# Kernel tuning notes

Hardware: AMD Instinct MI355X
Metric: run time of the kernel (lower is better)

## Reference

```python
import jax, jax.numpy as jnp
import numpy as np

EPS = 1e-5

def _conv(x, w, pad):
    # NCHW / OIHW 2-D convolution, stride 1
    return jax.lax.conv_general_dilated(
        x, w, window_strides=(1, 1), padding=[(pad, pad), (pad, pad)],
        dimension_numbers=('NCHW', 'OIHW', 'NCHW'))

def _bn2d(x, g, b, m, v):
    inv = g * jax.lax.rsqrt(v + EPS)
    return x * inv[None, :, None, None] + (b - m * inv)[None, :, None, None]

def _bn1d(x, g, b, m, v):
    inv = g * jax.lax.rsqrt(v + EPS)
    return x * inv[None, :] + (b - m * inv)[None, :]

def _avgpool2(x):
    B, C, H, W = x.shape
    return x.reshape(B, C, H // 2, 2, W // 2, 2).mean(axis=(3, 5))

def _hardtanh01(x):
    return jnp.clip(x, 0.0, 1.0)

def setup_inputs() -> dict:
    key = jax.random.key(0)
    ks = jax.random.split(key, 24)
    B = 1024
    d = {}
    d['x_in'] = jax.random.normal(ks[0], (B, 3, 32, 32), dtype=jnp.float32)
    d['w1'] = jax.random.normal(ks[1], (32, 3, 5, 5), dtype=jnp.float32) * 0.1
    d['w2'] = jax.random.normal(ks[2], (32, 32, 5, 5), dtype=jnp.float32) * 0.05
    d['w3'] = jax.random.normal(ks[3], (64, 32, 5, 5), dtype=jnp.float32) * 0.05
    d['w4'] = jax.random.normal(ks[4], (10, 64, 4, 4), dtype=jnp.float32) * 0.05
    for i, (c, k0) in enumerate([(32, 5), (32, 9), (64, 13), (10, 17)], start=1):
        d[f'g{i}'] = jax.random.uniform(ks[k0], (c,), minval=0.5, maxval=1.5, dtype=jnp.float32)
        d[f'b{i}'] = jax.random.normal(ks[k0 + 1], (c,), dtype=jnp.float32) * 0.1
        d[f'm{i}'] = jax.random.normal(ks[k0 + 2], (c,), dtype=jnp.float32) * 0.1
        d[f'v{i}'] = jax.random.uniform(ks[k0 + 3], (c,), minval=0.5, maxval=1.5, dtype=jnp.float32)
    return d

def reference(x_in, w1, w2, w3, w4,
              g1, b1, m1, v1, g2, b2, m2, v2,
              g3, b3, m3, v3, g4, b4, m4, v4):
    # conv1 -> bn1 -> pool -> hardtanh(0,1)
    x = _hardtanh01(_avgpool2(_bn2d(_conv(x_in, w1, 2), g1, b1, m1, v1)))
    # conv2 -> bn2 -> pool -> hardtanh(0,1)
    x = _hardtanh01(_avgpool2(_bn2d(_conv(x, w2, 2), g2, b2, m2, v2)))
    # conv3 -> bn3 -> pool -> hardtanh(0,1)
    x = _hardtanh01(_avgpool2(_bn2d(_conv(x, w3, 2), g3, b3, m3, v3)))
    # fc1 as 4x4 conv, valid padding -> (B, num_classes, 1, 1)
    x = _conv(x, w4, 0).reshape(x.shape[0], -1)
    return _bn1d(x, g4, b4, m4, v4)
```

## Files before the change

kernel.cpp:

```cpp
#include <hip/hip_runtime.h>

#define EPSF 1e-5f

typedef _Float16 half8 __attribute__((ext_vector_type(8)));
typedef _Float16 half4v __attribute__((ext_vector_type(4)));
typedef float f32x4 __attribute__((ext_vector_type(4)));

__device__ __forceinline__ float clamp01(float x){ return fminf(fmaxf(x, 0.f), 1.f); }

__global__ __launch_bounds__(256) void k_prep(
    const float* __restrict__ w1, const float* __restrict__ w2,
    const float* __restrict__ w3, const float* __restrict__ w4,
    const float* __restrict__ g1, const float* __restrict__ b1, const float* __restrict__ m1, const float* __restrict__ v1,
    const float* __restrict__ g2, const float* __restrict__ b2, const float* __restrict__ m2, const float* __restrict__ v2,
    const float* __restrict__ g3, const float* __restrict__ b3, const float* __restrict__ m3, const float* __restrict__ v3,
    const float* __restrict__ g4, const float* __restrict__ b4, const float* __restrict__ m4, const float* __restrict__ v4,
    _Float16* __restrict__ w1h, _Float16* __restrict__ w2h, _Float16* __restrict__ w3h,
    _Float16* __restrict__ w4h, float* __restrict__ bnc)
{
  const int t = blockIdx.x*256 + threadIdx.x;
  if (t < 5120) {
    int oc = t / 160, k = t - oc*160;
    int dy = k >> 5, rem = k & 31, dx = rem >> 2, ic = rem & 3;
    float val = (dx < 5 && ic < 3) ? w1[(oc*3+ic)*25 + dy*5 + dx] : 0.f;
    w1h[t] = (_Float16)val;
  }
  for (int i = t; i < 25600; i += 32768) {
    int tap = i >> 10, r = i & 1023, oc = r >> 5, ic = r & 31;
    w2h[i] = (_Float16)w2[(oc*32+ic)*25 + tap];
  }
  for (int i = t; i < 51200; i += 32768) {
    int tap = i >> 11, r = i & 2047, oc = r >> 5, ic = r & 31;
    w3h[i] = (_Float16)w3[(oc*32+ic)*25 + tap];
  }
  for (int i = t; i < 16384; i += 32768) {
    int oc = i >> 10, k = i & 1023, pos = k >> 6, ic = k & 63;
    float val = (oc < 10) ? w4[(oc*64+ic)*16 + pos] : 0.f;
    w4h[i] = (_Float16)val;
  }
  if (t < 32) {
    float inv = g1[t] / sqrtf(v1[t] + EPSF);
    bnc[t] = 0.25f*inv; bnc[32+t] = b1[t] - m1[t]*inv;
    float i2 = g2[t] / sqrtf(v2[t] + EPSF);
    bnc[64+t] = 0.25f*i2; bnc[96+t] = b2[t] - m2[t]*i2;
  }
  if (t < 64) {
    float i3 = g3[t] / sqrtf(v3[t] + EPSF);
    bnc[128+t] = 0.25f*i3; bnc[192+t] = b3[t] - m3[t]*i3;
  }
  if (t < 10) {
    float i4 = g4[t] / sqrtf(v4[t] + EPSF);
    bnc[256+t] = i4; bnc[266+t] = b4[t] - m4[t]*i4;
  }
}

__global__ __launch_bounds__(256) void k_fused(
    const float* __restrict__ x,
    const _Float16* __restrict__ w1h, const _Float16* __restrict__ w2h,
    const _Float16* __restrict__ w3h, const _Float16* __restrict__ w4h,
    const float* __restrict__ bnc, float* __restrict__ out)
{
  __shared__ __align__(16) char arena[45312];
  float*     P   = (float*)(arena);
  _Float16*  Bx1 = (_Float16*)(arena + 20736);
  _Float16*  Ip  = (_Float16*)(arena);
  _Float16*  Bx2 = (_Float16*)(arena + 16384);
  _Float16*  Ip2 = (_Float16*)(arena);
  _Float16*  Bx3 = (_Float16*)(arena + 4096);
  _Float16*  Ip3 = (_Float16*)(arena + 13776);
  float*     S4P = (float*)(arena + 15824);

  const int img = blockIdx.x;
  const int tid = threadIdx.x;
  const int w   = __builtin_amdgcn_readfirstlane(tid >> 6);
  const int l   = tid & 63;
  const int row = l & 15;
  const int kg  = l >> 4;

  for (int i = tid; i < 1928; i += 256)
    ((float4*)arena)[i] = make_float4(0.f,0.f,0.f,0.f);
  __syncthreads();
  {
    const float* xin = x + img*3072;
    #pragma unroll
    for (int rpt = 0; rpt < 3; ++rpt) {
      int i = tid + rpt*256;
      int ic = i >> 8, rem = i & 255;
      int y = rem >> 3, xq = rem & 7;
      float4 val = *(const float4*)(xin + ic*1024 + y*32 + xq*4);
      float* dst = P + ((y+2)*36 + xq*4 + 2)*4 + ic;
      dst[0]  = val.x; dst[4]  = val.y; dst[8]  = val.z; dst[12] = val.w;
    }
  }
  __syncthreads();

  for (int j = tid; j < 1225; j += 256) {
    int y = j / 35, xx = j - y*35;
    const float* p0 = P + (y*36 + xx)*4;
    float4 a = *(const float4*)(p0);
    float4 b = *(const float4*)(p0 + 4);
    float4 c = *(const float4*)(p0 + 144);
    float4 d = *(const float4*)(p0 + 148);
    half4v h;
    h[0] = (_Float16)((a.x + b.x) + (c.x + d.x));
    h[1] = (_Float16)((a.y + b.y) + (c.y + d.y));
    h[2] = (_Float16)((a.z + b.z) + (c.z + d.z));
    h[3] = (_Float16)((a.w + b.w) + (c.w + d.w));
    *(half4v*)(Bx1 + y*144 + xx*4) = h;
  }
  __syncthreads();

  {
    half8 B1[5][2];
    #pragma unroll
    for (int dy = 0; dy < 5; ++dy)
      #pragma unroll
      for (int nt = 0; nt < 2; ++nt)
        B1[dy][nt] = *(const half8*)(w1h + (nt*16 + row)*160 + dy*32 + kg*8);

    f32x4 acc[4][2];
    #pragma unroll
    for (int mt = 0; mt < 4; ++mt) { acc[mt][0] = (f32x4){0,0,0,0}; acc[mt][1] = (f32x4){0,0,0,0}; }

    #pragma unroll
    for (int mt = 0; mt < 4; ++mt) {
      const int py = w*4 + mt;
      #pragma unroll
      for (int dy = 0; dy < 5; ++dy) {
        half8 av = *(const half8*)(Bx1 + (2*py + dy)*144 + 8*row + 8*kg);
        acc[mt][0] = __builtin_amdgcn_mfma_f32_16x16x32_f16(av, B1[dy][0], acc[mt][0], 0, 0, 0);
        acc[mt][1] = __builtin_amdgcn_mfma_f32_16x16x32_f16(av, B1[dy][1], acc[mt][1], 0, 0, 0);
      }
    }
    __syncthreads();
    const float s0 = bnc[row],      h0 = bnc[32 + row];
    const float s1 = bnc[16 + row], h1 = bnc[48 + row];
    #pragma unroll
    for (int mt = 0; mt < 4; ++mt) {
      #pragma unroll
      for (int r = 0; r < 4; ++r) {
        int pix = (w*4 + mt)*16 + (l>>4)*4 + r;
        Ip[pix*32 + row]      = (_Float16)clamp01(fmaf(acc[mt][0][r], s0, h0));
        Ip[pix*32 + 16 + row] = (_Float16)clamp01(fmaf(acc[mt][1][r], s1, h1));
      }
    }
  }
  __syncthreads();

  {
    const half8* ip = (const half8*)Ip;
    for (int j = tid; j < 1444; j += 256) {
      int pos = j >> 2, g = j & 3;
      int y = pos / 19, xx = pos - y*19;
      int u = y - 2, v = xx - 2;
      bool r0 = (u >= 0) & (u < 16), r1 = (u >= -1) & (u < 15);
      bool c0 = (v >= 0) & (v < 16), c1 = (v >= -1) & (v < 15);
      half8 z = (half8)(_Float16)0.f;
      half8 a = z, b = z, c = z, d = z;
      if (r0 & c0) a = ip[(u*16+v)*4 + g];
      if (r0 & c1) b = ip[(u*16+v+1)*4 + g];
      if (r1 & c0) c = ip[((u+1)*16+v)*4 + g];
      if (r1 & c1) d = ip[((u+1)*16+v+1)*4 + g];
      half8 s = (a + b) + (c + d);
      *(half8*)(Bx2 + pos*40 + g*8) = s;
    }
  }
  __syncthreads();

  {
    const int p = w*16 + row, py = p >> 3, px = p & 7;
    const _Float16* BxBase = Bx2 + ((2*py)*19 + 2*px)*40 + kg*8;
    const _Float16* wbase  = w2h + row*32 + kg*8;
    f32x4 acc0 = {0,0,0,0}, acc1 = {0,0,0,0};
    half8 c0 = *(const half8*)(wbase);
    half8 c1 = *(const half8*)(wbase + 512);
    #pragma unroll
    for (int dy = 0; dy < 5; ++dy)
      #pragma unroll
      for (int dx = 0; dx < 5; ++dx) {
        const int tap = dy*5 + dx;
        const int tn  = (tap < 24) ? tap + 1 : 24;
        half8 n0 = *(const half8*)(wbase + tn*1024);
        half8 n1 = *(const half8*)(wbase + tn*1024 + 512);
        half8 av = *(const half8*)(BxBase + (dy*19 + dx)*40);
        acc0 = __builtin_amdgcn_mfma_f32_16x16x32_f16(av, c0, acc0, 0, 0, 0);
        acc1 = __builtin_amdgcn_mfma_f32_16x16x32_f16(av, c1, acc1, 0, 0, 0);
        c0 = n0; c1 = n1;
      }
    __syncthreads();
    const float s0 = bnc[64 + row],      h0 = bnc[96 + row];
    const float s1 = bnc[64 + 16 + row], h1 = bnc[96 + 16 + row];
    #pragma unroll
    for (int r = 0; r < 4; ++r) {
      int p2 = w*16 + (l >> 4)*4 + r;
      Ip2[p2*32 + row]      = (_Float16)clamp01(fmaf(acc0[r], s0, h0));
      Ip2[p2*32 + 16 + row] = (_Float16)clamp01(fmaf(acc1[r], s1, h1));
    }
  }
  __syncthreads();

  {
    const half8* ip = (const half8*)Ip2;
    for (int j = tid; j < 484; j += 256) {
      int pos = j >> 2, g = j & 3;
      int y = pos / 11, xx = pos - y*11;
      int u = y - 2, v = xx - 2;
      bool r0 = (u >= 0) & (u < 8), r1 = (u >= -1) & (u < 7);
      bool c0 = (v >= 0) & (v < 8), c1 = (v >= -1) & (v < 7);
      half8 z = (half8)(_Float16)0.f;
      half8 a = z, b = z, c = z, d = z;
      if (r0 & c0) a = ip[(u*8+v)*4 + g];
      if (r0 & c1) b = ip[(u*8+v+1)*4 + g];
      if (r1 & c0) c = ip[((u+1)*8+v)*4 + g];
      if (r1 & c1) d = ip[((u+1)*8+v+1)*4 + g];
      half8 s = (a + b) + (c + d);
      *(half8*)(Bx3 + pos*40 + g*8) = s;
    }
  }
  __syncthreads();

  {
    const int py = row >> 2, px = row & 3;
    const _Float16* BxBase = Bx3 + ((2*py)*11 + 2*px)*40 + kg*8;
    const _Float16* wbase  = w3h + (w*16 + row)*32 + kg*8;
    f32x4 acc = {0,0,0,0};
    half8 cb = *(const half8*)(wbase);
    #pragma unroll
    for (int dy = 0; dy < 5; ++dy)
      #pragma unroll
      for (int dx = 0; dx < 5; ++dx) {
        const int tap = dy*5 + dx;
        const int tn  = (tap < 24) ? tap + 1 : 24;
        half8 nb = *(const half8*)(wbase + tn*2048);
        half8 av = *(const half8*)(BxBase + (dy*11 + dx)*40);
        acc = __builtin_amdgcn_mfma_f32_16x16x32_f16(av, cb, acc, 0, 0, 0);
        cb = nb;
      }
    const int oc = w*16 + row;
    const float s3 = bnc[128 + oc], h3 = bnc[192 + oc];
    #pragma unroll
    for (int r = 0; r < 4; ++r) {
      int pix = (l >> 4)*4 + r;
      Ip3[pix*64 + oc] = (_Float16)clamp01(fmaf(acc[r], s3, h3));
    }
  }
  __syncthreads();

  if (tid < 160) {
    const int oc = tid >> 4, pix = tid & 15;
    const _Float16* A = Ip3 + pix*64;
    const _Float16* W = w4h + oc*1024 + pix*64;
    float a = 0.f;
    #pragma unroll
    for (int q = 0; q < 8; ++q) {
      half8 xa = *(const half8*)(A + q*8);
      half8 wv = *(const half8*)(W + q*8);
      #pragma unroll
      for (int j = 0; j < 8; ++j)
        a = fmaf((float)xa[j], (float)wv[j], a);
    }
    S4P[tid] = a;
  }
  __syncthreads();
  if (tid < 10) {
    float s = 0.f;
    #pragma unroll
    for (int i = 0; i < 16; ++i) s += S4P[tid*16 + i];
    out[img*10 + tid] = fmaf(s, bnc[256 + tid], bnc[266 + tid]);
  }
}

extern "C" void kernel_launch(void* const* d_in, const int* in_sizes, int n_in,
                              void* d_out, int out_size, void* d_ws, size_t ws_size,
                              hipStream_t stream)
{
  const float* x  = (const float*)d_in[0];
  const float* w1 = (const float*)d_in[1];
  const float* w2 = (const float*)d_in[2];
  const float* w3 = (const float*)d_in[3];
  const float* w4 = (const float*)d_in[4];
  const float *g1=(const float*)d_in[5],  *b1=(const float*)d_in[6],
              *m1=(const float*)d_in[7],  *v1=(const float*)d_in[8];
  const float *g2=(const float*)d_in[9],  *b2=(const float*)d_in[10],
              *m2=(const float*)d_in[11], *v2=(const float*)d_in[12];
  const float *g3=(const float*)d_in[13], *b3=(const float*)d_in[14],
              *m3=(const float*)d_in[15], *v3=(const float*)d_in[16];
  const float *g4=(const float*)d_in[17], *b4=(const float*)d_in[18],
              *m4=(const float*)d_in[19], *v4=(const float*)d_in[20];
  float* out = (float*)d_out;

  char* ws = (char*)d_ws;
  _Float16* w1h = (_Float16*)(ws);
  _Float16* w2h = (_Float16*)(ws + 10240);
  _Float16* w3h = (_Float16*)(ws + 61440);
  _Float16* w4h = (_Float16*)(ws + 163840);
  float*    bnc = (float*)   (ws + 196608);

  k_prep<<<dim3(128), dim3(256), 0, stream>>>(w1, w2, w3, w4,
      g1,b1,m1,v1, g2,b2,m2,v2, g3,b3,m3,v3, g4,b4,m4,v4,
      w1h, w2h, w3h, w4h, bnc);
  k_fused<<<dim3(1024), dim3(256), 0, stream>>>(x, w1h, w2h, w3h, w4h, bnc, out);
}
```

Baseline: 134.9 us.

## Fuse pooling box-sums into conv loads and shrink LDS for higher occupancy

```diff
diff --git a/kernel.cpp b/kernel.cpp
--- a/kernel.cpp
+++ b/kernel.cpp
@@ -54,21 +54,18 @@
   }
 }
 
-__global__ __launch_bounds__(256) void k_fused(
+__global__ __launch_bounds__(256, 4) void k_fused(
     const float* __restrict__ x,
     const _Float16* __restrict__ w1h, const _Float16* __restrict__ w2h,
     const _Float16* __restrict__ w3h, const _Float16* __restrict__ w4h,
     const float* __restrict__ bnc, float* __restrict__ out)
 {
-  __shared__ __align__(16) char arena[45312];
-  float*     P   = (float*)(arena);
-  _Float16*  Bx1 = (_Float16*)(arena + 20736);
-  _Float16*  Ip  = (_Float16*)(arena);
-  _Float16*  Bx2 = (_Float16*)(arena + 16384);
-  _Float16*  Ip2 = (_Float16*)(arena);
-  _Float16*  Bx3 = (_Float16*)(arena + 4096);
-  _Float16*  Ip3 = (_Float16*)(arena + 13776);
-  float*     S4P = (float*)(arena + 15824);
+  __shared__ __align__(16) char arena[32000];
+  _Float16* Bx1 = (_Float16*)arena;
+  _Float16* P2  = (_Float16*)arena;
+  _Float16* P3  = (_Float16*)arena;
+  _Float16* Ip3 = (_Float16*)(arena + 11520);
+  float*    S4P = (float*)(arena + 13568);
 
   const int img = blockIdx.x;
   const int tid = threadIdx.x;
@@ -77,172 +74,176 @@
   const int row = l & 15;
   const int kg  = l >> 4;
 
-  for (int i = tid; i < 1928; i += 256)
-    ((float4*)arena)[i] = make_float4(0.f,0.f,0.f,0.f);
-  __syncthreads();
   {
     const float* xin = x + img*3072;
-    #pragma unroll
-    for (int rpt = 0; rpt < 3; ++rpt) {
-      int i = tid + rpt*256;
-      int ic = i >> 8, rem = i & 255;
-      int y = rem >> 3, xq = rem & 7;
-      float4 val = *(const float4*)(xin + ic*1024 + y*32 + xq*4);
-      float* dst = P + ((y+2)*36 + xq*4 + 2)*4 + ic;
-      dst[0]  = val.x; dst[4]  = val.y; dst[8]  = val.z; dst[12] = val.w;
-    }
-  }
-  __syncthreads();
-
-  for (int j = tid; j < 1225; j += 256) {
-    int y = j / 35, xx = j - y*35;
-    const float* p0 = P + (y*36 + xx)*4;
-    float4 a = *(const float4*)(p0);
-    float4 b = *(const float4*)(p0 + 4);
-    float4 c = *(const float4*)(p0 + 144);
-    float4 d = *(const float4*)(p0 + 148);
-    half4v h;
-    h[0] = (_Float16)((a.x + b.x) + (c.x + d.x));
-    h[1] = (_Float16)((a.y + b.y) + (c.y + d.y));
-    h[2] = (_Float16)((a.z + b.z) + (c.z + d.z));
-    h[3] = (_Float16)((a.w + b.w) + (c.w + d.w));
-    *(half4v*)(Bx1 + y*144 + xx*4) = h;
-  }
-  __syncthreads();
-
+    for (int j = tid; j < 1330; j += 256) {
+      int y = j / 38, xx = j - y*38;
+      float s0 = 0.f, s1 = 0.f, s2 = 0.f;
+      #pragma unroll
+      for (int r = 0; r < 2; ++r) {
+        int iy = y - 2 + r;
+        if ((unsigned)iy < 32u) {
+          #pragma unroll
+          for (int c = 0; c < 2; ++c) {
+            int ix = xx - 2 + c;
+            if ((unsigned)ix < 32u) {
+              int o = iy*32 + ix;
+              s0 += xin[o]; s1 += xin[1024 + o]; s2 += xin[2048 + o];
+            }
+          }
+        }
+      }
+      half4v h; h[0] = (_Float16)s0; h[1] = (_Float16)s1; h[2] = (_Float16)s2; h[3] = (_Float16)0.f;
+      *(half4v*)(Bx1 + y*160 + xx*4) = h;
+    }
+  }
+  __syncthreads();
+
+  f32x4 acc1[4][2];
   {
     half8 B1[5][2];
     #pragma unroll
-    for (int dy = 0; dy < 5; ++dy)
-      #pragma unroll
-      for (int nt = 0; nt < 2; ++nt)
-        B1[dy][nt] = *(const half8*)(w1h + (nt*16 + row)*160 + dy*32 + kg*8);
-
-    f32x4 acc[4][2];
-    #pragma unroll
-    for (int mt = 0; mt < 4; ++mt) { acc[mt][0] = (f32x4){0,0,0,0}; acc[mt][1] = (f32x4){0,0,0,0}; }
-
+    for (int dy = 0; dy < 5; ++dy) {
+      B1[dy][0] = *(const half8*)(w1h + row*160 + dy*32 + kg*8);
+      B1[dy][1] = *(const half8*)(w1h + (16 + row)*160 + dy*32 + kg*8);
+    }
+    #pragma unroll
+    for (int mt = 0; mt < 4; ++mt) { acc1[mt][0] = (f32x4){0,0,0,0}; acc1[mt][1] = (f32x4){0,0,0,0}; }
+    const int xoff = 8*(row + kg);
     #pragma unroll
     for (int mt = 0; mt < 4; ++mt) {
       const int py = w*4 + mt;
       #pragma unroll
       for (int dy = 0; dy < 5; ++dy) {
-        half8 av = *(const half8*)(Bx1 + (2*py + dy)*144 + 8*row + 8*kg);
-        acc[mt][0] = __builtin_amdgcn_mfma_f32_16x16x32_f16(av, B1[dy][0], acc[mt][0], 0, 0, 0);
-        acc[mt][1] = __builtin_amdgcn_mfma_f32_16x16x32_f16(av, B1[dy][1], acc[mt][1], 0, 0, 0);
-      }
-    }
-    __syncthreads();
+        half8 av = *(const half8*)(Bx1 + (2*py + dy)*160 + xoff);
+        acc1[mt][0] = __builtin_amdgcn_mfma_f32_16x16x32_f16(av, B1[dy][0], acc1[mt][0], 0, 0, 0);
+        acc1[mt][1] = __builtin_amdgcn_mfma_f32_16x16x32_f16(av, B1[dy][1], acc1[mt][1], 0, 0, 0);
+      }
+    }
+  }
+  __syncthreads();
+
+  for (int j = tid; j < 1600; j += 256) {
+    int u = j & 3, pos = j >> 2;
+    int a = pos/20, c = pos - a*20;
+    bool interior = ((unsigned)(a-2) < 16u) & ((unsigned)(c-2) < 16u);
+    if (!interior) *(half8*)(P2 + pos*40 + u*8) = (half8)(_Float16)0.f;
+  }
+  {
     const float s0 = bnc[row],      h0 = bnc[32 + row];
     const float s1 = bnc[16 + row], h1 = bnc[48 + row];
     #pragma unroll
     for (int mt = 0; mt < 4; ++mt) {
+      const int py = w*4 + mt;
       #pragma unroll
       for (int r = 0; r < 4; ++r) {
-        int pix = (w*4 + mt)*16 + (l>>4)*4 + r;
-        Ip[pix*32 + row]      = (_Float16)clamp01(fmaf(acc[mt][0][r], s0, h0));
-        Ip[pix*32 + 16 + row] = (_Float16)clamp01(fmaf(acc[mt][1][r], s1, h1));
-      }
-    }
-  }
-  __syncthreads();
-
-  {
-    const half8* ip = (const half8*)Ip;
-    for (int j = tid; j < 1444; j += 256) {
-      int pos = j >> 2, g = j & 3;
-      int y = pos / 19, xx = pos - y*19;
-      int u = y - 2, v = xx - 2;
-      bool r0 = (u >= 0) & (u < 16), r1 = (u >= -1) & (u < 15);
-      bool c0 = (v >= 0) & (v < 16), c1 = (v >= -1) & (v < 15);
-      half8 z = (half8)(_Float16)0.f;
-      half8 a = z, b = z, c = z, d = z;
-      if (r0 & c0) a = ip[(u*16+v)*4 + g];
-      if (r0 & c1) b = ip[(u*16+v+1)*4 + g];
-      if (r1 & c0) c = ip[((u+1)*16+v)*4 + g];
-      if (r1 & c1) d = ip[((u+1)*16+v+1)*4 + g];
-      half8 s = (a + b) + (c + d);
-      *(half8*)(Bx2 + pos*40 + g*8) = s;
-    }
-  }
-  __syncthreads();
-
-  {
-    const int p = w*16 + row, py = p >> 3, px = p & 7;
-    const _Float16* BxBase = Bx2 + ((2*py)*19 + 2*px)*40 + kg*8;
-    const _Float16* wbase  = w2h + row*32 + kg*8;
-    f32x4 acc0 = {0,0,0,0}, acc1 = {0,0,0,0};
-    half8 c0 = *(const half8*)(wbase);
-    half8 c1 = *(const half8*)(wbase + 512);
-    #pragma unroll
-    for (int dy = 0; dy < 5; ++dy)
+        int pcol = kg*4 + r;
+        int idx = ((py+2)*20 + pcol+2)*40;
+        P2[idx + row]      = (_Float16)clamp01(fmaf(acc1[mt][0][r], s0, h0));
+        P2[idx + 16 + row] = (_Float16)clamp01(fmaf(acc1[mt][1][r], s1, h1));
+      }
+    }
+  }
+  __syncthreads();
+
+  f32x4 a2_0 = {0,0,0,0}, a2_1 = {0,0,0,0};
+  {
+    const int pixel = w*16 + row;
+    const int py = pixel >> 3, px = pixel & 7;
+    const _Float16* base = P2 + ((2*py)*20 + 2*px)*40 + kg*8;
+    half8 RA[6], RB[6];
+    #pragma unroll
+    for (int c = 0; c < 6; ++c) RA[c] = *(const half8*)(base + c*40);
+    #pragma unroll
+    for (int c = 0; c < 6; ++c) RB[c] = *(const half8*)(base + 800 + c*40);
+    const _Float16* wb = w2h + row*32 + kg*8;
+    half8 cw0 = *(const half8*)(wb);
+    half8 cw1 = *(const half8*)(wb + 512);
+    #pragma unroll
+    for (int dy = 0; dy < 5; ++dy) {
+      half8 cs[6];
+      #pragma unroll
+      for (int c = 0; c < 6; ++c) cs[c] = RA[c] + RB[c];
+      if (dy < 4) {
+        #pragma unroll
+        for (int c = 0; c < 6; ++c) {
+          half8 nv = *(const half8*)(base + (dy+2)*800 + c*40);
+          if ((dy & 1) == 0) RA[c] = nv; else RB[c] = nv;
+        }
+      }
       #pragma unroll
       for (int dx = 0; dx < 5; ++dx) {
         const int tap = dy*5 + dx;
-        const int tn  = (tap < 24) ? tap + 1 : 24;
-        half8 n0 = *(const half8*)(wbase + tn*1024);
-        half8 n1 = *(const half8*)(wbase + tn*1024 + 512);
-        half8 av = *(const half8*)(BxBase + (dy*19 + dx)*40);
-        acc0 = __builtin_amdgcn_mfma_f32_16x16x32_f16(av, c0, acc0, 0, 0, 0);
-        acc1 = __builtin_amdgcn_mfma_f32_16x16x32_f16(av, c1, acc1, 0, 0, 0);
-        c0 = n0; c1 = n1;
-      }
-    __syncthreads();
-    const float s0 = bnc[64 + row],      h0 = bnc[96 + row];
-    const float s1 = bnc[64 + 16 + row], h1 = bnc[96 + 16 + row];
+        const int tn = (tap < 24) ? tap + 1 : 24;
+        half8 nw0 = *(const half8*)(wb + tn*1024);
+        half8 nw1 = *(const half8*)(wb + tn*1024 + 512);
+        half8 av = cs[dx] + cs[dx+1];
+        a2_0 = __builtin_amdgcn_mfma_f32_16x16x32_f16(av, cw0, a2_0, 0, 0, 0);
+        a2_1 = __builtin_amdgcn_mfma_f32_16x16x32_f16(av, cw1, a2_1, 0, 0, 0);
+        cw0 = nw0; cw1 = nw1;
+      }
+    }
+  }
+  __syncthreads();
+
+  for (int j = tid; j < 576; j += 256) {
+    int u = j & 3, pos = j >> 2;
+    int a = pos/12, c = pos - a*12;
+    bool interior = ((unsigned)(a-2) < 8u) & ((unsigned)(c-2) < 8u);
+    if (!interior) *(half8*)(P3 + pos*40 + u*8) = (half8)(_Float16)0.f;
+  }
+  {
+    const float s0 = bnc[64 + row], h0 = bnc[96 + row];
+    const float s1 = bnc[80 + row], h1 = bnc[112 + row];
     #pragma unroll
     for (int r = 0; r < 4; ++r) {
-      int p2 = w*16 + (l >> 4)*4 + r;
-      Ip2[p2*32 + row]      = (_Float16)clamp01(fmaf(acc0[r], s0, h0));
-      Ip2[p2*32 + 16 + row] = (_Float16)clamp01(fmaf(acc1[r], s1, h1));
-    }
-  }
-  __syncthreads();
-
-  {
-    const half8* ip = (const half8*)Ip2;
-    for (int j = tid; j < 484; j += 256) {
-      int pos = j >> 2, g = j & 3;
-      int y = pos / 11, xx = pos - y*11;
-      int u = y - 2, v = xx - 2;
-      bool r0 = (u >= 0) & (u < 8), r1 = (u >= -1) & (u < 7);
-      bool c0 = (v >= 0) & (v < 8), c1 = (v >= -1) & (v < 7);
-      half8 z = (half8)(_Float16)0.f;
-      half8 a = z, b = z, c = z, d = z;
-      if (r0 & c0) a = ip[(u*8+v)*4 + g];
-      if (r0 & c1) b = ip[(u*8+v+1)*4 + g];
-      if (r1 & c0) c = ip[((u+1)*8+v)*4 + g];
-      if (r1 & c1) d = ip[((u+1)*8+v+1)*4 + g];
-      half8 s = (a + b) + (c + d);
-      *(half8*)(Bx3 + pos*40 + g*8) = s;
+      int p2 = w*16 + kg*4 + r;
+      int py2 = p2 >> 3, px2 = p2 & 7;
+      int idx = ((py2+2)*12 + px2+2)*40;
+      P3[idx + row]      = (_Float16)clamp01(fmaf(a2_0[r], s0, h0));
+      P3[idx + 16 + row] = (_Float16)clamp01(fmaf(a2_1[r], s1, h1));
     }
   }
   __syncthreads();
 
   {
     const int py = row >> 2, px = row & 3;
-    const _Float16* BxBase = Bx3 + ((2*py)*11 + 2*px)*40 + kg*8;
-    const _Float16* wbase  = w3h + (w*16 + row)*32 + kg*8;
-    f32x4 acc = {0,0,0,0};
-    half8 cb = *(const half8*)(wbase);
-    #pragma unroll
-    for (int dy = 0; dy < 5; ++dy)
+    const _Float16* base = P3 + ((2*py)*12 + 2*px)*40 + kg*8;
+    half8 RA[6], RB[6];
+    #pragma unroll
+    for (int c = 0; c < 6; ++c) RA[c] = *(const half8*)(base + c*40);
+    #pragma unroll
+    for (int c = 0; c < 6; ++c) RB[c] = *(const half8*)(base + 480 + c*40);
+    const _Float16* wb = w3h + (w*16 + row)*32 + kg*8;
+    half8 cw = *(const half8*)(wb);
+    f32x4 a3 = {0,0,0,0};
+    #pragma unroll
+    for (int dy = 0; dy < 5; ++dy) {
+      half8 cs[6];
+      #pragma unroll
+      for (int c = 0; c < 6; ++c) cs[c] = RA[c] + RB[c];
+      if (dy < 4) {
+        #pragma unroll
+        for (int c = 0; c < 6; ++c) {
+          half8 nv = *(const half8*)(base + (dy+2)*480 + c*40);
+          if ((dy & 1) == 0) RA[c] = nv; else RB[c] = nv;
+        }
+      }
       #pragma unroll
       for (int dx = 0; dx < 5; ++dx) {
         const int tap = dy*5 + dx;
-        const int tn  = (tap < 24) ? tap + 1 : 24;
-        half8 nb = *(const half8*)(wbase + tn*2048);
-        half8 av = *(const half8*)(BxBase + (dy*11 + dx)*40);
-        acc = __builtin_amdgcn_mfma_f32_16x16x32_f16(av, cb, acc, 0, 0, 0);
-        cb = nb;
-      }
+        const int tn = (tap < 24) ? tap + 1 : 24;
+        half8 nw = *(const half8*)(wb + tn*2048);
+        half8 av = cs[dx] + cs[dx+1];
+        a3 = __builtin_amdgcn_mfma_f32_16x16x32_f16(av, cw, a3, 0, 0, 0);
+        cw = nw;
+      }
+    }
     const int oc = w*16 + row;
     const float s3 = bnc[128 + oc], h3 = bnc[192 + oc];
     #pragma unroll
-    for (int r = 0; r < 4; ++r) {
-      int pix = (l >> 4)*4 + r;
-      Ip3[pix*64 + oc] = (_Float16)clamp01(fmaf(acc[r], s3, h3));
-    }
+    for (int r = 0; r < 4; ++r)
+      Ip3[(kg*4 + r)*64 + oc] = (_Float16)clamp01(fmaf(a3[r], s3, h3));
   }
   __syncthreads();
 
```

Result: faster. 129.9 us (-3.7%).
